# Optimization experiments

Measured on AMD Instinct MI355X. Metric: run time of the kernel, lower is better.

The kernel has to match this reference:

```python
import jax, jax.numpy as jnp
import numpy as np

LOG2 = 0.6931471805599453
GAMMA = 10.0
NUM_KERNELS = 301
N_LAYERS = 3


def ssp(v):
    # ShiftedSoftplus: softplus(x) - log(2)
    return jax.nn.softplus(v) - jnp.asarray(LOG2, v.dtype)


def setup_inputs() -> dict:
    key = jax.random.key(0)
    ks = jax.random.split(key, 20)
    N, F, K, L, V = 512, 128, NUM_KERNELS, N_LAYERS, 100
    s = 0.05
    return {
        "x": jax.random.randint(ks[0], (N,), 0, V),
        "r": jax.random.uniform(ks[1], (N, 3), dtype=jnp.float32) * 10.0,
        "emb": jax.random.normal(ks[2], (V, F), dtype=jnp.float32),
        "aw_W": jax.random.normal(ks[3], (L, F, F), dtype=jnp.float32) * s,
        "aw_b": jax.random.normal(ks[4], (L, F), dtype=jnp.float32) * s,
        "cf_W1": jax.random.normal(ks[5], (L, K, F), dtype=jnp.float32) * s,
        "cf_b1": jax.random.normal(ks[6], (L, F), dtype=jnp.float32) * s,
        "cf_W2": jax.random.normal(ks[7], (L, F, F), dtype=jnp.float32) * s,
        "cf_b2": jax.random.normal(ks[8], (L, F), dtype=jnp.float32) * s,
        "n_W1": jax.random.normal(ks[9], (L, F, F), dtype=jnp.float32) * s,
        "n_b1": jax.random.normal(ks[10], (L, F), dtype=jnp.float32) * s,
        "n_W2": jax.random.normal(ks[11], (L, F, F), dtype=jnp.float32) * s,
        "n_b2": jax.random.normal(ks[12], (L, F), dtype=jnp.float32) * s,
        "out_W1": jax.random.normal(ks[13], (F, 32), dtype=jnp.float32) * s,
        "out_b1": jax.random.normal(ks[14], (32,), dtype=jnp.float32) * s,
        "out_W2": jax.random.normal(ks[15], (32, 1), dtype=jnp.float32) * s,
        "out_b2": jax.random.normal(ks[16], (1,), dtype=jnp.float32) * s,
    }


def reference(x, r, emb, aw_W, aw_b, cf_W1, cf_b1, cf_W2, cf_b2,
              n_W1, n_b1, n_W2, n_b2, out_W1, out_b1, out_W2, out_b2):
    centers = jnp.linspace(0.0, 30.0, NUM_KERNELS, dtype=r.dtype)  # [K]
    # pairwise distances (torch.cdist, p=2) with safe sqrt at the diagonal
    diff = r[:, None, :] - r[None, :, :]                 # [N,N,3]
    d2 = jnp.sum(diff * diff, axis=-1)                   # [N,N]
    mask = d2 > 0
    d = jnp.where(mask, jnp.sqrt(jnp.where(mask, d2, 1.0)), 0.0)

    h = emb[x]                                           # [N,F]
    for l in range(N_LAYERS):
        o = h @ aw_W[l] + aw_b[l]                        # atom-wise linear
        # Gaussian RBF expansion: [N,N,K]
        e = jnp.exp(-GAMMA * jnp.square(d[..., None] - centers))
        # filter-generating MLP: [N,N,F]
        w = ssp(e @ cf_W1[l] + cf_b1[l])
        w = ssp(w @ cf_W2[l] + cf_b2[l])
        # continuous-filter conv: o[i,k] = sum_j x[j,k] * w[i,j,k]
        c = jnp.einsum('jk,ijk->ik', o, w)
        c = ssp(c @ n_W1[l] + n_b1[l]) @ n_W2[l] + n_b2[l]
        h = h + c
    out = ssp(h @ out_W1 + out_b1) @ out_W2 + out_b2     # [N,1]
    # AdaptiveAvgPool1d(1) on a 2D [N,1] tensor is identity over L=1
    return out.reshape(-1)
```

## Files before the change

kernel.cpp:

```cpp
#include <hip/hip_runtime.h>
#include <hip/hip_fp16.h>
#include <math.h>

#define N_ATOMS 512
#define F_DIM   128
#define K_RBF   301
#define NLAYER  3
#define GAMMA_C 10.0f
#define LOG2_C  0.6931471805599453f

#define TAB_H     0.01f
#define TAB_INVH  100.0f
#define TAB_ROWS  1768
#define RPB       8
#define NGROUPS   (TAB_ROWS / RPB)
#define NTASKS    (NGROUPS * NLAYER)
#define NBBLK2    ((NTASKS + 1) / 2)
#define ROW_BYTES 512

#define JSPLIT  4
#define JPB     (N_ATOMS / JSPLIT)

__device__ __forceinline__ float ssp(float x) {
    float ax = fabsf(x);
    return fmaxf(x, 0.0f) + log1pf(expf(-ax)) - LOG2_C;
}
__device__ __forceinline__ __half2 u2h2(unsigned u) {
    union { unsigned u; __half2 h; } c; c.u = u; return c.h;
}
__device__ __forceinline__ unsigned h22u(__half2 h) {
    union { unsigned u; __half2 h; } c; c.h = h; return c.u;
}

__global__ void __launch_bounds__(256)
prep_build(const int* __restrict__ x, const float* __restrict__ r,
           const float* __restrict__ emb,
           const float* __restrict__ aw_W, const float* __restrict__ aw_b,
           const float* __restrict__ cf_W1, const float* __restrict__ cf_b1,
           const float* __restrict__ cf_W2, const float* __restrict__ cf_b2,
           uint2* __restrict__ dpk, float* __restrict__ h,
           unsigned* __restrict__ opk, uint2* __restrict__ ptab) {
    __shared__ float hs[F_DIM];
    __shared__ float os[F_DIM];
    __shared__ float red2[2 * F_DIM];
    __shared__ float e_s[2][RPB + 1][34];
    __shared__ float w1_s[2][F_DIM][12];

    if (blockIdx.x < N_ATOMS) {
        int i = blockIdx.x;
        int t = threadIdx.x;
        float rx = r[i * 3 + 0], ry = r[i * 3 + 1], rz = r[i * 3 + 2];
        if (t < F_DIM) {
            float hv = emb[x[i] * F_DIM + t];
            h[i * F_DIM + t] = hv;
            hs[t] = hv;
        }
        for (int j = t; j < N_ATOMS; j += 256) {
            float dx = rx - r[j * 3 + 0];
            float dy = ry - r[j * 3 + 1];
            float dz = rz - r[j * 3 + 2];
            float d  = sqrtf(dx * dx + dy * dy + dz * dz);
            float xb = d * TAB_INVH;
            int   b  = ::min((int)xb, TAB_ROWS - 2);
            float fr = xb - (float)b;
            __half fh = __float2half(fr);
            dpk[i * N_ATOMS + j] = make_uint2((unsigned)b * ROW_BYTES,
                                              h22u(__halves2half2(fh, fh)));
        }
        __syncthreads();
        {
            int q = t >> 7, f = t & 127;
            float a = 0.0f;
            int g0 = q * 64;
            for (int g = 0; g < 64; ++g)
                a = fmaf(hs[g0 + g], aw_W[(g0 + g) * F_DIM + f], a);
            red2[q * F_DIM + f] = a;
        }
        __syncthreads();
        if (t < F_DIM) os[t] = red2[t] + red2[F_DIM + t] + aw_b[t];
        __syncthreads();
        if (t < F_DIM / 2)
            opk[i * 64 + t] = h22u(__halves2half2(__float2half(os[2 * t]),
                                                  __float2half(os[2 * t + 1])));
        return;
    }

    int u = threadIdx.x >> 7;
    int f = threadIdx.x & 127;
    int task = (blockIdx.x - N_ATOMS) * 2 + u;
    bool valid = task < NTASKS;
    task = valid ? task : NTASKS - 1;
    int l    = task / NGROUPS;
    int row0 = (task % NGROUPS) * RPB;

    float dlo = row0 * TAB_H;
    float dhi = (row0 + RPB) * TAB_H;
    int k0 = ::max(0, (int)ceilf((dlo - 1.45f) * 10.0f));
    int k1 = ::min(K_RBF - 1, (int)floorf((dhi + 1.45f) * 10.0f));
    int kw = k1 - k0 + 1;

    for (int idx = f; idx < (RPB + 1) * kw; idx += F_DIM) {
        int rr = idx / kw, kk = idx % kw;
        float dv = (row0 + rr) * TAB_H;
        float tt = dv - 0.1f * (float)(k0 + kk);
        e_s[u][rr][kk] = expf(-GAMMA_C * tt * tt);
    }
    __syncthreads();

    const float* W1 = cf_W1 + l * K_RBF * F_DIM;
    float b1v = cf_b1[l * F_DIM + f];
    float acc[RPB + 1];
#pragma unroll
    for (int rr = 0; rr <= RPB; ++rr) acc[rr] = b1v;
    for (int kk = 0; kk < kw; ++kk) {
        float w1v = W1[(k0 + kk) * F_DIM + f];
#pragma unroll
        for (int rr = 0; rr <= RPB; ++rr) acc[rr] = fmaf(e_s[u][rr][kk], w1v, acc[rr]);
    }
#pragma unroll
    for (int rr = 0; rr <= RPB; ++rr) w1_s[u][f][rr] = ssp(acc[rr]);
    __syncthreads();

    const float* W2 = cf_W2 + l * F_DIM * F_DIM;
    float b2v = cf_b2[l * F_DIM + f];
    float acc2[RPB + 1];
#pragma unroll
    for (int rr = 0; rr <= RPB; ++rr) acc2[rr] = b2v;
    for (int g = 0; g < F_DIM; ++g) {
        float w2v = W2[g * F_DIM + f];
        float4 wa = *(const float4*)&w1_s[u][g][0];
        float4 wb = *(const float4*)&w1_s[u][g][4];
        float  wc = w1_s[u][g][8];
        acc2[0] = fmaf(wa.x, w2v, acc2[0]);
        acc2[1] = fmaf(wa.y, w2v, acc2[1]);
        acc2[2] = fmaf(wa.z, w2v, acc2[2]);
        acc2[3] = fmaf(wa.w, w2v, acc2[3]);
        acc2[4] = fmaf(wb.x, w2v, acc2[4]);
        acc2[5] = fmaf(wb.y, w2v, acc2[5]);
        acc2[6] = fmaf(wb.z, w2v, acc2[6]);
        acc2[7] = fmaf(wb.w, w2v, acc2[7]);
        acc2[8] = fmaf(wc,   w2v, acc2[8]);
    }
    float o9[RPB + 1];
#pragma unroll
    for (int rr = 0; rr <= RPB; ++rr) o9[rr] = ssp(acc2[rr]);

    if (valid) {
        int p = f >> 1;
        bool odd = (f & 1);
#pragma unroll
        for (int rr = 0; rr < RPB; ++rr) {
            float t0 = o9[rr];
            float dt = o9[rr + 1] - o9[rr];
            float ot0 = __shfl_xor(t0, 1, 64);
            float odt = __shfl_xor(dt, 1, 64);
            if (!odd) {
                uint2 v = make_uint2(
                    h22u(__halves2half2(__float2half(t0), __float2half(ot0))),
                    h22u(__halves2half2(__float2half(dt), __float2half(odt))));
                ptab[((size_t)l * TAB_ROWS + row0 + rr) * 64 + p] = v;
            }
        }
    }
}

__global__ void __launch_bounds__(256, 8)
conv_kernel(const uint2* __restrict__ dpk, const unsigned* __restrict__ opk_in,
            const uint2* __restrict__ ptab, float* __restrict__ c_part, int l) {
    int bid = blockIdx.x;
    int i = bid >> 2;
    int q = bid & 3;
    int t = threadIdx.x;
    int p2 = t & 31;
    int jc = t >> 5;

    __shared__ __align__(16) uint2 ds[JPB];
    __shared__ __align__(16) float redbuf[8 * 32 * 4];

    if (t < JPB) ds[t] = dpk[i * N_ATOMS + q * JPB + t];
    __syncthreads();

    const char*  T  = (const char*)(ptab + (size_t)l * TAB_ROWS * 64) + p2 * 16;
    const uint2* ob = (const uint2*)opk_in + p2 + (size_t)(q * JPB) * 32;

    float4 acc = make_float4(0.0f, 0.0f, 0.0f, 0.0f);
    int j0 = jc * 16;
#pragma unroll 4
    for (int jj = 0; jj < 16; ++jj) {
        int j = j0 + jj;
        uint2 e = ds[j];
        uint4 tv = *(const uint4*)(T + e.x);
        uint2 ohu = ob[j * 32];
        __half2 fr2 = u2h2(e.y);
        __half2 wa = __hfma2(fr2, u2h2(tv.y), u2h2(tv.x));
        __half2 wb = __hfma2(fr2, u2h2(tv.w), u2h2(tv.z));
        __half2 oa = u2h2(ohu.x);
        __half2 obh = u2h2(ohu.y);
        acc.x = fmaf(__half2float(__low2half(wa)),  __half2float(__low2half(oa)),  acc.x);
        acc.y = fmaf(__half2float(__high2half(wa)), __half2float(__high2half(oa)), acc.y);
        acc.z = fmaf(__half2float(__low2half(wb)),  __half2float(__low2half(obh)), acc.z);
        acc.w = fmaf(__half2float(__high2half(wb)), __half2float(__high2half(obh)), acc.w);
    }
    *(float4*)&redbuf[(jc * 32 + p2) * 4] = acc;
    __syncthreads();
    if (t < 32) {
        float4 s = *(const float4*)&redbuf[t * 4];
#pragma unroll
        for (int qq = 1; qq < 8; ++qq) {
            float4 v = *(const float4*)&redbuf[(qq * 32 + t) * 4];
            s.x += v.x; s.y += v.y; s.z += v.z; s.w += v.w;
        }
        *(float4*)&c_part[((size_t)(i * JSPLIT + q)) * F_DIM + 4 * t] = s;
    }
}

__global__ void __launch_bounds__(512)
node_kernel(const float* __restrict__ c_part,
            const float* __restrict__ n_W1, const float* __restrict__ n_b1,
            const float* __restrict__ n_W2, const float* __restrict__ n_b2,
            float* __restrict__ h,
            const float* __restrict__ aw_W, const float* __restrict__ aw_b,
            unsigned* __restrict__ opk_out,
            const float* __restrict__ oW1, const float* __restrict__ ob1,
            const float* __restrict__ oW2, const float* __restrict__ ob2,
            float* __restrict__ out, int l) {
    int i = blockIdx.x;
    int t = threadIdx.x;

    __shared__ __align__(16) float cs[F_DIM];
    __shared__ __align__(16) float t1s[F_DIM];
    __shared__ __align__(16) float hs[F_DIM];
    __shared__ __align__(16) float redbuf[4 * F_DIM];

    if (t < F_DIM) {
        const float* cp = c_part + (size_t)i * JSPLIT * F_DIM + t;
        cs[t] = (cp[0] + cp[F_DIM]) + (cp[2 * F_DIM] + cp[3 * F_DIM]);
        hs[t] = h[i * F_DIM + t];
    }
    __syncthreads();

    {
        int q = t >> 7, f = t & 127;
        const float* W1 = n_W1 + l * F_DIM * F_DIM;
        float a = 0.0f;
        int g0 = q * 32;
        for (int g = 0; g < 32; ++g) a = fmaf(cs[g0 + g], W1[(g0 + g) * F_DIM + f], a);
        redbuf[q * F_DIM + f] = a;
    }
    __syncthreads();
    if (t < F_DIM)
        t1s[t] = ssp((redbuf[t] + redbuf[F_DIM + t])
                   + (redbuf[2 * F_DIM + t] + redbuf[3 * F_DIM + t])
                   + n_b1[l * F_DIM + t]);
    __syncthreads();

    {
        int q = t >> 7, f = t & 127;
        const float* W2 = n_W2 + l * F_DIM * F_DIM;
        float a = 0.0f;
        int g0 = q * 32;
        for (int g = 0; g < 32; ++g) a = fmaf(t1s[g0 + g], W2[(g0 + g) * F_DIM + f], a);
        redbuf[q * F_DIM + f] = a;
    }
    __syncthreads();
    if (t < F_DIM) {
        float hv = hs[t] + (redbuf[t] + redbuf[F_DIM + t])
                         + (redbuf[2 * F_DIM + t] + redbuf[3 * F_DIM + t])
                         + n_b2[l * F_DIM + t];
        hs[t] = hv;
        if (l < NLAYER - 1) h[i * F_DIM + t] = hv;
    }
    __syncthreads();

    if (l < NLAYER - 1) {
        {
            int q = t >> 7, f = t & 127;
            const float* W = aw_W + (l + 1) * F_DIM * F_DIM;
            float a = 0.0f;
            int g0 = q * 32;
            for (int g = 0; g < 32; ++g) a = fmaf(hs[g0 + g], W[(g0 + g) * F_DIM + f], a);
            redbuf[q * F_DIM + f] = a;
        }
        __syncthreads();
        if (t < F_DIM) {
            t1s[t] = (redbuf[t] + redbuf[F_DIM + t])
                   + (redbuf[2 * F_DIM + t] + redbuf[3 * F_DIM + t])
                   + aw_b[(l + 1) * F_DIM + t];
        }
        __syncthreads();
        if (t < F_DIM / 2)
            opk_out[i * 64 + t] = h22u(__halves2half2(__float2half(t1s[2 * t]),
                                                      __float2half(t1s[2 * t + 1])));
    } else {
        {
            int q = t >> 5, f = t & 31;
            float a = 0.0f;
            int g0 = q * 8;
            for (int g = 0; g < 8; ++g) a = fmaf(hs[g0 + g], oW1[(g0 + g) * 32 + f], a);
            redbuf[q * 32 + f] = a;
        }
        __syncthreads();
        float val = 0.0f;
        if (t < 32) {
            float a = ob1[t];
#pragma unroll
            for (int q = 0; q < 16; ++q) a += redbuf[q * 32 + t];
            val = ssp(a) * oW2[t];
        }
#pragma unroll
        for (int off = 16; off > 0; off >>= 1) val += __shfl_xor(val, off, 64);
        if (t == 0) out[i] = val + ob2[0];
    }
}

extern "C" void kernel_launch(void* const* d_in, const int* in_sizes, int n_in,
                              void* d_out, int out_size, void* d_ws, size_t ws_size,
                              hipStream_t stream) {
    const int*   x     = (const int*)  d_in[0];
    const float* r     = (const float*)d_in[1];
    const float* emb   = (const float*)d_in[2];
    const float* aw_W  = (const float*)d_in[3];
    const float* aw_b  = (const float*)d_in[4];
    const float* cf_W1 = (const float*)d_in[5];
    const float* cf_b1 = (const float*)d_in[6];
    const float* cf_W2 = (const float*)d_in[7];
    const float* cf_b2 = (const float*)d_in[8];
    const float* n_W1  = (const float*)d_in[9];
    const float* n_b1  = (const float*)d_in[10];
    const float* n_W2  = (const float*)d_in[11];
    const float* n_b2  = (const float*)d_in[12];
    const float* oW1   = (const float*)d_in[13];
    const float* ob1   = (const float*)d_in[14];
    const float* oW2   = (const float*)d_in[15];
    const float* ob2   = (const float*)d_in[16];
    float* out = (float*)d_out;

    char* ws = (char*)d_ws;
    uint2*    dpk    = (uint2*)ws;    ws += (size_t)N_ATOMS * N_ATOMS * 8;
    float*    h      = (float*)ws;    ws += (size_t)N_ATOMS * F_DIM * 4;
    unsigned* opkA   = (unsigned*)ws; ws += (size_t)N_ATOMS * (F_DIM / 2) * 4;
    unsigned* opkB   = (unsigned*)ws; ws += (size_t)N_ATOMS * (F_DIM / 2) * 4;
    uint2*    ptab   = (uint2*)ws;    ws += (size_t)NLAYER * TAB_ROWS * 64 * 8;
    float*    c_part = (float*)ws;

    prep_build<<<N_ATOMS + NBBLK2, 256, 0, stream>>>(
        x, r, emb, aw_W, aw_b, cf_W1, cf_b1, cf_W2, cf_b2, dpk, h, opkA, ptab);
    for (int l = 0; l < NLAYER; ++l) {
        unsigned* oin  = (l & 1) ? opkB : opkA;
        unsigned* oout = (l & 1) ? opkA : opkB;
        conv_kernel<<<N_ATOMS * JSPLIT, 256, 0, stream>>>(dpk, oin, ptab, c_part, l);
        node_kernel<<<N_ATOMS, 512, 0, stream>>>(
            c_part, n_W1, n_b1, n_W2, n_b2, h, aw_W, aw_b, oout,
            oW1, ob1, oW2, ob2, out, l);
    }
}
```

Baseline: 158.8 us.

## Split table-build reductions across two half-blocks, one task per block

The filter-table build part of prep_build now gives each 256-thread block a single task instead of two. The two 128-thread halves split the K reduction of the first MLP layer and the F reduction of the second layer, then combine partial sums through shared memory. This doubles the block count and shortens each thread's serial FMA chain, aiming to cut the latency of this phase. The cost is extra syncthreads and shared-memory reduction traffic, and only half the threads do the ssp and pack steps.

```diff
diff --git a/kernel.cpp b/kernel.cpp
--- a/kernel.cpp
+++ b/kernel.cpp
@@ -15,7 +15,6 @@
 #define RPB       8
 #define NGROUPS   (TAB_ROWS / RPB)
 #define NTASKS    (NGROUPS * NLAYER)
-#define NBBLK2    ((NTASKS + 1) / 2)
 #define ROW_BYTES 512
 
 #define JSPLIT  4
@@ -42,9 +41,9 @@
            unsigned* __restrict__ opk, uint2* __restrict__ ptab) {
     __shared__ float hs[F_DIM];
     __shared__ float os[F_DIM];
-    __shared__ float red2[2 * F_DIM];
-    __shared__ float e_s[2][RPB + 1][34];
-    __shared__ float w1_s[2][F_DIM][12];
+    __shared__ float red2[2][F_DIM][10];
+    __shared__ float e_s[RPB + 1][34];
+    __shared__ float w1_s[F_DIM][12];
 
     if (blockIdx.x < N_ATOMS) {
         int i = blockIdx.x;
@@ -74,10 +73,10 @@
             int g0 = q * 64;
             for (int g = 0; g < 64; ++g)
                 a = fmaf(hs[g0 + g], aw_W[(g0 + g) * F_DIM + f], a);
-            red2[q * F_DIM + f] = a;
-        }
-        __syncthreads();
-        if (t < F_DIM) os[t] = red2[t] + red2[F_DIM + t] + aw_b[t];
+            red2[q][f][0] = a;
+        }
+        __syncthreads();
+        if (t < F_DIM) os[t] = red2[0][t][0] + red2[1][t][0] + aw_b[t];
         __syncthreads();
         if (t < F_DIM / 2)
             opk[i * 64 + t] = h22u(__halves2half2(__float2half(os[2 * t]),
@@ -85,11 +84,10 @@
         return;
     }
 
-    int u = threadIdx.x >> 7;
-    int f = threadIdx.x & 127;
-    int task = (blockIdx.x - N_ATOMS) * 2 + u;
-    bool valid = task < NTASKS;
-    task = valid ? task : NTASKS - 1;
+    int t = threadIdx.x;
+    int v = t >> 7;
+    int f = t & 127;
+    int task = blockIdx.x - N_ATOMS;
     int l    = task / NGROUPS;
     int row0 = (task % NGROUPS) * RPB;
 
@@ -99,55 +97,68 @@
     int k1 = ::min(K_RBF - 1, (int)floorf((dhi + 1.45f) * 10.0f));
     int kw = k1 - k0 + 1;
 
-    for (int idx = f; idx < (RPB + 1) * kw; idx += F_DIM) {
+    for (int idx = t; idx < (RPB + 1) * kw; idx += 256) {
         int rr = idx / kw, kk = idx % kw;
         float dv = (row0 + rr) * TAB_H;
         float tt = dv - 0.1f * (float)(k0 + kk);
-        e_s[u][rr][kk] = expf(-GAMMA_C * tt * tt);
+        e_s[rr][kk] = expf(-GAMMA_C * tt * tt);
     }
     __syncthreads();
 
     const float* W1 = cf_W1 + l * K_RBF * F_DIM;
-    float b1v = cf_b1[l * F_DIM + f];
     float acc[RPB + 1];
 #pragma unroll
-    for (int rr = 0; rr <= RPB; ++rr) acc[rr] = b1v;
-    for (int kk = 0; kk < kw; ++kk) {
+    for (int rr = 0; rr <= RPB; ++rr) acc[rr] = 0.0f;
+    for (int kk = v; kk < kw; kk += 2) {
         float w1v = W1[(k0 + kk) * F_DIM + f];
 #pragma unroll
-        for (int rr = 0; rr <= RPB; ++rr) acc[rr] = fmaf(e_s[u][rr][kk], w1v, acc[rr]);
-    }
-#pragma unroll
-    for (int rr = 0; rr <= RPB; ++rr) w1_s[u][f][rr] = ssp(acc[rr]);
+        for (int rr = 0; rr <= RPB; ++rr) acc[rr] = fmaf(e_s[rr][kk], w1v, acc[rr]);
+    }
+#pragma unroll
+    for (int rr = 0; rr <= RPB; ++rr) red2[v][f][rr] = acc[rr];
+    __syncthreads();
+    if (t < F_DIM) {
+        float b1v = cf_b1[l * F_DIM + t];
+#pragma unroll
+        for (int rr = 0; rr <= RPB; ++rr)
+            w1_s[t][rr] = ssp(red2[0][t][rr] + red2[1][t][rr] + b1v);
+    }
     __syncthreads();
 
     const float* W2 = cf_W2 + l * F_DIM * F_DIM;
-    float b2v = cf_b2[l * F_DIM + f];
     float acc2[RPB + 1];
 #pragma unroll
-    for (int rr = 0; rr <= RPB; ++rr) acc2[rr] = b2v;
-    for (int g = 0; g < F_DIM; ++g) {
-        float w2v = W2[g * F_DIM + f];
-        float4 wa = *(const float4*)&w1_s[u][g][0];
-        float4 wb = *(const float4*)&w1_s[u][g][4];
-        float  wc = w1_s[u][g][8];
-        acc2[0] = fmaf(wa.x, w2v, acc2[0]);
-        acc2[1] = fmaf(wa.y, w2v, acc2[1]);
-        acc2[2] = fmaf(wa.z, w2v, acc2[2]);
-        acc2[3] = fmaf(wa.w, w2v, acc2[3]);
-        acc2[4] = fmaf(wb.x, w2v, acc2[4]);
-        acc2[5] = fmaf(wb.y, w2v, acc2[5]);
-        acc2[6] = fmaf(wb.z, w2v, acc2[6]);
-        acc2[7] = fmaf(wb.w, w2v, acc2[7]);
-        acc2[8] = fmaf(wc,   w2v, acc2[8]);
-    }
-    float o9[RPB + 1];
-#pragma unroll
-    for (int rr = 0; rr <= RPB; ++rr) o9[rr] = ssp(acc2[rr]);
-
-    if (valid) {
-        int p = f >> 1;
-        bool odd = (f & 1);
+    for (int rr = 0; rr <= RPB; ++rr) acc2[rr] = 0.0f;
+    {
+        int g0 = v * 64;
+        for (int g = g0; g < g0 + 64; ++g) {
+            float w2v = W2[g * F_DIM + f];
+            float4 wa = *(const float4*)&w1_s[g][0];
+            float4 wb = *(const float4*)&w1_s[g][4];
+            float  wc = w1_s[g][8];
+            acc2[0] = fmaf(wa.x, w2v, acc2[0]);
+            acc2[1] = fmaf(wa.y, w2v, acc2[1]);
+            acc2[2] = fmaf(wa.z, w2v, acc2[2]);
+            acc2[3] = fmaf(wa.w, w2v, acc2[3]);
+            acc2[4] = fmaf(wb.x, w2v, acc2[4]);
+            acc2[5] = fmaf(wb.y, w2v, acc2[5]);
+            acc2[6] = fmaf(wb.z, w2v, acc2[6]);
+            acc2[7] = fmaf(wb.w, w2v, acc2[7]);
+            acc2[8] = fmaf(wc,   w2v, acc2[8]);
+        }
+    }
+#pragma unroll
+    for (int rr = 0; rr <= RPB; ++rr) red2[v][f][rr] = acc2[rr];
+    __syncthreads();
+    if (t < F_DIM) {
+        float b2v = cf_b2[l * F_DIM + t];
+        float o9[RPB + 1];
+#pragma unroll
+        for (int rr = 0; rr <= RPB; ++rr)
+            o9[rr] = ssp(red2[0][t][rr] + red2[1][t][rr] + b2v);
+
+        int p = t >> 1;
+        bool odd = (t & 1);
 #pragma unroll
         for (int rr = 0; rr < RPB; ++rr) {
             float t0 = o9[rr];
@@ -155,10 +166,10 @@
             float ot0 = __shfl_xor(t0, 1, 64);
             float odt = __shfl_xor(dt, 1, 64);
             if (!odd) {
-                uint2 v = make_uint2(
+                uint2 vv = make_uint2(
                     h22u(__halves2half2(__float2half(t0), __float2half(ot0))),
                     h22u(__halves2half2(__float2half(dt), __float2half(odt))));
-                ptab[((size_t)l * TAB_ROWS + row0 + rr) * 64 + p] = v;
+                ptab[((size_t)l * TAB_ROWS + row0 + rr) * 64 + p] = vv;
             }
         }
     }
@@ -343,7 +354,7 @@
     uint2*    ptab   = (uint2*)ws;    ws += (size_t)NLAYER * TAB_ROWS * 64 * 8;
     float*    c_part = (float*)ws;
 
-    prep_build<<<N_ATOMS + NBBLK2, 256, 0, stream>>>(
+    prep_build<<<N_ATOMS + NTASKS, 256, 0, stream>>>(
         x, r, emb, aw_W, aw_b, cf_W1, cf_b1, cf_W2, cf_b2, dpk, h, opkA, ptab);
     for (int l = 0; l < NLAYER; ++l) {
         unsigned* oin  = (l & 1) ? opkB : opkA;
```

Result: no change. 157.4 us (-0.9%).
